# Performance work log

Hardware: AMD Instinct MI355X
Metric: run time of the kernel (lower is better)

The kernel has to match this reference:

```python
import jax, jax.numpy as jnp
import numpy as np

K = 5        # spline kernel_size per dim (dim=2 -> 25 kernel weights)
NPG = 75     # MNIST superpixel nodes per graph


def _spline_conv(x, src, dst, pseudo, emask, W, root, bias):
    """SplineConv, dim=2, kernel_size=5, degree=1 open splines, aggr='mean'.
    emask in {0,1} masks out coalesced-away (duplicate/self-loop) edges."""
    n = x.shape[0]
    v = jnp.clip(pseudo, 0.0, 1.0) * (K - 1)
    bot = jnp.clip(jnp.floor(v), 0, K - 2)
    frac = v - bot                                   # [E,2]
    bot = bot.astype(jnp.int32)
    xj = x[src] * emask[:, None]                     # [E,Fin] gathered source feats
    # aggregate-then-transform: acc[k,i,:] = sum over edges into i with basis k
    acc = jnp.zeros((K * K, n, x.shape[1]), x.dtype)
    for o0 in (0, 1):
        for o1 in (0, 1):
            w = (frac[:, 0] if o0 else 1.0 - frac[:, 0]) * (frac[:, 1] if o1 else 1.0 - frac[:, 1])
            kk = (bot[:, 0] + o0) + K * (bot[:, 1] + o1)
            acc = acc.at[kk, dst].add(w[:, None] * xj)
    out = jnp.einsum('knf,kfo->no', acc, W)
    deg = jax.ops.segment_sum(emask, dst, num_segments=n)
    return out / jnp.maximum(deg, 1.0)[:, None] + x @ root + bias


def _pool(x, pos, valid, batch, src, dst, emask, size, G, B):
    """voxel_grid + max_pool with static shapes: S=B*G*G clusters, masked."""
    S = B * G * G
    c = jnp.clip(jnp.floor(pos / size).astype(jnp.int32), 0, G - 1)
    cl = batch * (G * G) + c[:, 1] * G + c[:, 0]
    xm = jnp.where(valid[:, None] > 0, x, -1e30)
    px = jax.ops.segment_max(xm, cl, num_segments=S)
    cnt = jax.ops.segment_sum(valid, cl, num_segments=S)
    sval = (cnt > 0).astype(x.dtype)
    px = jnp.where(sval[:, None] > 0, px, 0.0)
    ppos = jax.ops.segment_sum(pos * valid[:, None], cl, num_segments=S) / jnp.maximum(cnt, 1.0)[:, None]
    nb = jnp.arange(S, dtype=jnp.int32) // (G * G)
    # remap edges to clusters; mask self loops and duplicates (= coalesce)
    nsrc, ndst = cl[src], cl[dst]
    m = (emask > 0) & (nsrc != ndst)
    a0 = jnp.where(m, nsrc, S)
    b0 = jnp.where(m, ndst, S)
    order = jnp.lexsort((b0, a0))
    a, b = a0[order], b0[order]
    first = jnp.concatenate([jnp.array([True]), (a[1:] != a[:-1]) | (b[1:] != b[:-1])])
    keep = jnp.zeros(src.shape[0], dtype=bool).at[order].set(first & (a < S))
    kf = keep.astype(x.dtype)
    # T.Cartesian(cat=False, norm=True): pseudo = (pos_src-pos_dst)/(2*max|.|)+0.5
    cart = ppos[nsrc] - ppos[ndst]
    amax = jnp.maximum(jnp.max(jnp.abs(cart) * kf[:, None]), 1e-12)
    pseudo = cart / (2.0 * amax) + 0.5
    return px, ppos, sval, nb, nsrc, ndst, kf, pseudo


def _forward(x, pos, src, dst, W1, r1, b1, W2, r2, b2, W3, r3, b3, fw1, fb1, fw2, fb2):
    N = x.shape[0]
    B = N // NPG
    batch = jnp.arange(N, dtype=jnp.int32) // NPG
    valid = jnp.ones((N,), x.dtype)
    emask = jnp.ones((src.shape[0],), x.dtype)
    cart = pos[src] - pos[dst]
    pseudo = cart / (2.0 * jnp.maximum(jnp.max(jnp.abs(cart)), 1e-12)) + 0.5
    x = jax.nn.elu(_spline_conv(x, src, dst, pseudo, emask, W1, r1, b1))
    x, pos, valid, batch, src, dst, emask, pseudo = _pool(x, pos, valid, batch, src, dst, emask, 5.0, 6, B)
    x = jax.nn.elu(_spline_conv(x, src, dst, pseudo, emask, W2, r2, b2))
    x, pos, valid, batch, src, dst, emask, pseudo = _pool(x, pos, valid, batch, src, dst, emask, 7.0, 5, B)
    x = jax.nn.elu(_spline_conv(x, src, dst, pseudo, emask, W3, r3, b3))
    # max_pool_x(cluster, x, batch, size=4): 2x2 voxel grid (size=14, end=27.99)
    c = jnp.clip(jnp.floor(pos / 14.0).astype(jnp.int32), 0, 1)
    cl = batch * 4 + c[:, 1] * 2 + c[:, 0]
    xm = jnp.where(valid[:, None] > 0, x, -1e30)
    px = jax.ops.segment_max(xm, cl, num_segments=B * 4)
    cnt = jax.ops.segment_sum(valid, cl, num_segments=B * 4)
    px = jnp.where((cnt > 0)[:, None], px, 0.0)
    h = jax.nn.elu(px.reshape(B, 4 * 64) @ fw1.T + fb1)
    logits = h @ fw2.T + fb2  # F.dropout is identity in eval mode
    return jax.nn.log_softmax(logits, axis=1)


def setup_inputs() -> dict:
    key = jax.random.key(0)
    ks = jax.random.split(key, 16)
    B, EPG = 1024, 1392
    N = B * NPG
    x = jax.random.normal(ks[0], (N, 1), jnp.float32)
    pos = jax.random.uniform(ks[1], (N, 2), jnp.float32) * 27.99
    s = jax.random.randint(ks[2], (B, EPG), 0, NPG)
    d = (s + 1 + jax.random.randint(ks[3], (B, EPG), 0, NPG - 1)) % NPG  # no self loops
    off = (jnp.arange(B, dtype=jnp.int32) * NPG)[:, None]
    src = (s + off).reshape(-1)
    dst = (d + off).reshape(-1)
    rn = lambda k, sh, sc: jax.random.normal(k, sh, jnp.float32) * sc
    return dict(x=x, pos=pos, src=src, dst=dst,
                W1=rn(ks[4], (25, 1, 32), 0.2), r1=rn(ks[5], (1, 32), 0.2), b1=jnp.zeros((32,), jnp.float32),
                W2=rn(ks[6], (25, 32, 64), 0.05), r2=rn(ks[7], (32, 64), 0.1), b2=jnp.zeros((64,), jnp.float32),
                W3=rn(ks[8], (25, 64, 64), 0.04), r3=rn(ks[9], (64, 64), 0.08), b3=jnp.zeros((64,), jnp.float32),
                fw1=rn(ks[10], (128, 256), 0.06), fb1=jnp.zeros((128,), jnp.float32),
                fw2=rn(ks[11], (10, 128), 0.09), fb2=jnp.zeros((10,), jnp.float32))


def reference(x, pos, src, dst, W1, r1, b1, W2, r2, b2, W3, r3, b3, fw1, fb1, fw2, fb2):
    return _forward(x, pos, src, dst, W1, r1, b1, W2, r2, b2, W3, r3, b3, fw1, fb1, fw2, fb2)
```

## Files before the change

kernel.cpp:

```cpp
#include <hip/hip_runtime.h>
#include <math.h>

#define NPG 75
#define KDIM 5

typedef _Float16 half8 __attribute__((ext_vector_type(8)));
typedef float f32x4 __attribute__((ext_vector_type(4)));

__device__ __forceinline__ float eluf(float v){ return v > 0.f ? v : expf(v) - 1.f; }

__device__ __forceinline__ void atomAddF(float* p, float v){ unsafeAtomicAdd(p, v); }

__device__ __forceinline__ unsigned fenc(float f){
    unsigned u = __float_as_uint(f);
    return (u & 0x80000000u) ? ~u : (u | 0x80000000u);
}
__device__ __forceinline__ float fdec(unsigned u){
    return (u & 0x80000000u) ? __uint_as_float(u & 0x7FFFFFFFu) : __uint_as_float(~u);
}

__device__ __forceinline__ void fma25(float (&r)[25], const float (&wx)[5], const float (&wyx)[5]){
    #pragma unroll
    for (int b1 = 0; b1 < 5; b1++)
        #pragma unroll
        for (int b0 = 0; b0 < 5; b0++)
            asm("v_fmac_f32 %0, %1, %2" : "+v"(r[b1 * 5 + b0]) : "v"(wx[b0]), "v"(wyx[b1]));
}

__device__ __forceinline__ void spline2(float c0, float c1, float am, int* kks, float* wsp){
    float denom = 2.f * fmaxf(am, 1e-12f);
    float p0 = c0 / denom + 0.5f;
    float p1 = c1 / denom + 0.5f;
    p0 = fminf(fmaxf(p0, 0.f), 1.f) * 4.f;
    p1 = fminf(fmaxf(p1, 0.f), 1.f) * 4.f;
    float b0 = fminf(floorf(p0), 3.f);
    float b1 = fminf(floorf(p1), 3.f);
    float f0 = p0 - b0, f1 = p1 - b1;
    int i0 = (int)b0, i1 = (int)b1;
    wsp[0] = (1.f - f0) * (1.f - f1); kks[0] = i0     + KDIM *  i1;
    wsp[1] =        f0  * (1.f - f1); kks[1] = i0 + 1 + KDIM *  i1;
    wsp[2] = (1.f - f0) *        f1 ; kks[2] = i0     + KDIM * (i1 + 1);
    wsp[3] =        f0  *        f1 ; kks[3] = i0 + 1 + KDIM * (i1 + 1);
}

__device__ __forceinline__ void spline_pay(float2 c, float denom, float* d){
    float p0 = fminf(fmaxf(c.x / denom + 0.5f, 0.f), 1.f) * 4.f;
    float p1 = fminf(fmaxf(c.y / denom + 0.5f, 0.f), 1.f) * 4.f;
    float b0 = fminf(floorf(p0), 3.f);
    float b1 = fminf(floorf(p1), 3.f);
    int i0 = (int)b0, i1 = (int)b1;
    float f0 = p0 - b0, f1 = p1 - b1;
    #pragma unroll
    for (int k = 0; k < 4; k++){
        d[k]     = (k == i0) ? (1.f - f0) : ((k == i0 + 1) ? f0 : 0.f);
        d[4 + k] = (k == i1) ? (1.f - f1) : ((k == i1 + 1) ? f1 : 0.f);
    }
}

__global__ __launch_bounds__(256) void amax0_k(
        const float* __restrict__ pos, const int* __restrict__ src,
        const int* __restrict__ dst, int E4, unsigned* __restrict__ outbits){
    float cand = 0.f;
    for (int i = blockIdx.x * 256 + threadIdx.x; i < E4; i += gridDim.x * 256){
        int4 s4 = ((const int4*)src)[i];
        int4 d4 = ((const int4*)dst)[i];
        #pragma unroll
        for (int k = 0; k < 4; k++){
            int s = (&s4.x)[k], d = (&d4.x)[k];
            float c0 = pos[s*2]   - pos[d*2];
            float c1 = pos[s*2+1] - pos[d*2+1];
            cand = fmaxf(cand, fmaxf(fabsf(c0), fabsf(c1)));
        }
    }
    __shared__ float sm[256];
    sm[threadIdx.x] = cand; __syncthreads();
    for (int o = 128; o > 0; o >>= 1){
        if (threadIdx.x < o) sm[threadIdx.x] = fmaxf(sm[threadIdx.x], sm[threadIdx.x + o]);
        __syncthreads();
    }
    if (threadIdx.x == 0) atomicMax(outbits, __float_as_uint(sm[0]));
}

__global__ __launch_bounds__(512) void conv1dedup_k(
        const float* __restrict__ x, const float* __restrict__ pos,
        const int* __restrict__ src, const int* __restrict__ dst, int EPG,
        const unsigned* __restrict__ amaxp,
        const float* __restrict__ W1, const float* __restrict__ r1, const float* __restrict__ b1,
        float* __restrict__ px1, float* __restrict__ pp1, float* __restrict__ sv1,
        int* __restrict__ easrc, float2* __restrict__ ecart,
        int* __restrict__ rowptr2, int* __restrict__ kcnt, unsigned* __restrict__ amaxbits){
    __shared__ __align__(16) float acc[NPG * 28];
    __shared__ float deg[NPG];
    __shared__ float xl[NPG], p0l[NPG], p1l[NPG];
    __shared__ int   cli[NPG];
    __shared__ float W1s[800], r1s[32], b1s[32];
    __shared__ unsigned px[36 * 32];
    __shared__ float cnt[36], ps[72], ppS[72];
    __shared__ unsigned pm[36 * 36];
    __shared__ float degs[36];
    __shared__ int rs[37], cur[36];
    __shared__ float red[8];
    __shared__ unsigned short sdS[2048];

    const int b = blockIdx.x, t = threadIdx.x;
    const int lane = t & 63, wid = t >> 6;
    const int n0 = b * NPG, e0 = b * EPG;

    const float am = __uint_as_float(*amaxp);

    for (int i = t; i < NPG * 28; i += 512) acc[i] = 0.f;
    for (int i = t; i < 36 * 32; i += 512) px[i] = 0u;
    for (int i = t; i < 36 * 36; i += 512) pm[i] = 0xFFFFFFFFu;
    if (t < NPG) deg[t] = 0.f;
    if (t < 36){ cnt[t] = 0.f; degs[t] = 0.f; }
    if (t < 72) ps[t] = 0.f;
    for (int i = t; i < 800; i += 512) W1s[i] = W1[i];
    if (t < 32){ r1s[t] = r1[t]; b1s[t] = b1[t]; }
    if (t < NPG){
        float p0 = pos[(n0 + t) * 2], p1 = pos[(n0 + t) * 2 + 1];
        xl[t] = x[n0 + t]; p0l[t] = p0; p1l[t] = p1;
        int c0 = min(max((int)floorf(p0 / 5.f), 0), 5);
        int c1 = min(max((int)floorf(p1 / 5.f), 0), 5);
        cli[t] = c1 * 6 + c0;
    }
    __syncthreads();

    if (t < NPG){
        int c = cli[t];
        atomAddF(&cnt[c], 1.f);
        atomAddF(&ps[c*2],     p0l[t]);
        atomAddF(&ps[c*2 + 1], p1l[t]);
    }
    #pragma unroll 4
    for (int it = 0; it < 4; it++){
        int e = t + it * 512;
        if (e < EPG){
            int s = src[e0 + e] - n0;
            int d = dst[e0 + e] - n0;
            sdS[e] = (unsigned short)(s | (d << 8));
            float c0 = p0l[s] - p0l[d];
            float c1 = p1l[s] - p1l[d];
            int kks[4]; float wsp[4];
            spline2(c0, c1, am, kks, wsp);
            float xv = xl[s];
            #pragma unroll
            for (int c = 0; c < 4; c++) atomAddF(&acc[d*28 + kks[c]], wsp[c] * xv);
            atomAddF(&deg[d], 1.f);
        }
    }
    __syncthreads();

    if (t < 36){
        float c = cnt[t], m = fmaxf(c, 1.f);
        float q0 = ps[t*2] / m, q1 = ps[t*2 + 1] / m;
        ppS[t*2] = q0; ppS[t*2 + 1] = q1;
        pp1[(b*36 + t)*2]     = q0;
        pp1[(b*36 + t)*2 + 1] = q1;
        sv1[b*36 + t] = (c > 0.f) ? 1.f : 0.f;
    }
    {
        const int o = t & 31;
        float wreg[25];
        #pragma unroll
        for (int k = 0; k < 25; k++) wreg[k] = W1s[k * 32 + o];
        const float rro = r1s[o], bbo = b1s[o];
        const int ii = t >> 5;
        #pragma unroll
        for (int r = 0; r < 5; r++){
            int i = ii + r * 16;
            if (i < NPG){
                const float4* ar = (const float4*)(acc + i * 28);
                float s = 0.f;
                #pragma unroll
                for (int q = 0; q < 7; q++){
                    float4 aq = ar[q];
                    s += aq.x * wreg[q*4];
                    if (q*4 + 1 < 25) s += aq.y * wreg[q*4 + 1];
                    if (q*4 + 2 < 25) s += aq.z * wreg[q*4 + 2];
                    if (q*4 + 3 < 25) s += aq.w * wreg[q*4 + 3];
                }
                float v = s / fmaxf(deg[i], 1.f) + xl[i] * rro + bbo;
                v = eluf(v);
                atomicMax(&px[cli[i]*32 + o], fenc(v));
            }
        }
    }
    int lab[4];
    #pragma unroll 4
    for (int it = 0; it < 4; it++){
        int e = t + it * 512;
        lab[it] = 0;
        if (e < EPG){
            int sd = (int)sdS[e];
            int a  = cli[sd & 255];
            int bb = cli[sd >> 8];
            lab[it] = a | (bb << 8) | ((a != bb) ? 0x10000 : 0);
            if (a != bb) atomicMin(&pm[a * 36 + bb], (unsigned)e);
        }
    }
    __syncthreads();

    for (int idx = t; idx < 36 * 32; idx += 512){
        int s_ = idx >> 5;
        px1[(size_t)(b*36)*32 + idx] = (cnt[s_] > 0.f) ? fdec(px[idx]) : 0.f;
    }
    float cand = 0.f;
    unsigned keptM = 0;
    #pragma unroll 4
    for (int it = 0; it < 4; it++){
        int e = t + it * 512;
        int L = lab[it];
        if (L & 0x10000){
            int a = L & 255, bb = (L >> 8) & 255;
            if (pm[a * 36 + bb] == (unsigned)e){
                keptM |= 1u << it;
                atomAddF(&degs[bb], 1.f);
                float c0 = ppS[a*2]     - ppS[bb*2];
                float c1 = ppS[a*2 + 1] - ppS[bb*2 + 1];
                cand = fmaxf(cand, fmaxf(fabsf(c0), fabsf(c1)));
            }
        }
    }
    #pragma unroll
    for (int o = 1; o < 64; o <<= 1) cand = fmaxf(cand, __shfl_xor(cand, o, 64));
    if (lane == 0) red[wid] = cand;
    __syncthreads();
    if (t == 0){
        float m = red[0];
        #pragma unroll
        for (int i = 1; i < 8; i++) m = fmaxf(m, red[i]);
        atomicMax(amaxbits, __float_as_uint(m));
    }
    if (t < 64){
        int v = (t < 36) ? (int)degs[t] : 0;
        int incl = v;
        #pragma unroll
        for (int o = 1; o < 64; o <<= 1){
            int u = __shfl_up(incl, o, 64);
            if (t >= o) incl += u;
        }
        if (t == 0) rs[0] = 0;
        if (t < 36) rs[t + 1] = incl;
    }
    __syncthreads();
    if (t < 36){
        rowptr2[(b*36 + t)*2]     = e0 + rs[t];
        rowptr2[(b*36 + t)*2 + 1] = e0 + rs[t + 1];
        cur[t] = rs[t];
    }
    if (t == 0) kcnt[b] = rs[36];
    __syncthreads();
    #pragma unroll 4
    for (int it = 0; it < 4; it++){
        if (keptM & (1u << it)){
            int L = lab[it];
            int a = L & 255, bb = (L >> 8) & 255;
            int slot = atomicAdd(&cur[bb], 1);
            easrc[e0 + slot] = b*36 + a;
            ecart[e0 + slot] = make_float2(ppS[a*2] - ppS[bb*2], ppS[a*2 + 1] - ppS[bb*2 + 1]);
        }
    }
}

__global__ __launch_bounds__(1024) void dedup_pool_k(
        const int* __restrict__ easrc_in, const int* __restrict__ rowptr_in,
        const int* __restrict__ kcnt_in,
        const float* __restrict__ xin,
        const float* __restrict__ pp1, const float* __restrict__ sv1,
        int EPG,
        float* __restrict__ px2, float* __restrict__ pp2, float* __restrict__ sv2,
        int* __restrict__ easrc, float2* __restrict__ ecart,
        int* __restrict__ rowptr2, int* __restrict__ kcnt, unsigned* __restrict__ amaxbits){
    constexpr int GG = 25, NN = 36;
    __shared__ unsigned pm[GG * GG];
    __shared__ float degs[GG];
    __shared__ int rs[GG + 1];
    __shared__ int cur[GG];
    __shared__ float red[16];
    __shared__ int   clS[NN];
    __shared__ int   vld[NN];
    __shared__ int   rsS[NN + 1];
    __shared__ float ppS[2 * GG];
    __shared__ unsigned px[GG * 64];
    __shared__ float cnt[GG], ps[2 * GG];
    __shared__ unsigned short abS[1280];

    const int b = blockIdx.x, t = threadIdx.x;
    const int lane = t & 63, wid = t >> 6;
    const int e0 = b * EPG;
    const int cb25 = b * GG;
    const int nb36 = b * NN;

    for (int i = t; i < GG * GG; i += 1024) pm[i] = 0xFFFFFFFFu;
    for (int i = t; i < GG * 64; i += 1024) px[i] = 0u;
    if (t < GG){ degs[t] = 0.f; cnt[t] = 0.f; }
    if (t < 2 * GG) ps[t] = 0.f;
    if (t < NN){
        float v  = sv1[nb36 + t];
        float p0 = pp1[(nb36 + t)*2], p1 = pp1[(nb36 + t)*2 + 1];
        int c0 = min(max((int)floorf(p0 / 7.f), 0), 4);
        int c1 = min(max((int)floorf(p1 / 7.f), 0), 4);
        clS[t] = c1 * 5 + c0;
        vld[t] = (v > 0.f) ? 1 : 0;
        rsS[t] = rowptr_in[(nb36 + t)*2] - e0;
    }
    if (t == 0) rsS[NN] = kcnt_in[b];
    __syncthreads();

    const int kn = rsS[NN];

    if (t < NN && vld[t]){
        int c = clS[t];
        atomAddF(&cnt[c], 1.f);
        atomAddF(&ps[c*2],     pp1[(nb36 + t)*2]);
        atomAddF(&ps[c*2 + 1], pp1[(nb36 + t)*2 + 1]);
    }
    for (int idx = t; idx < NN * 64; idx += 1024){
        int i = idx >> 6, f = idx & 63;
        if (vld[i])
            atomicMax(&px[clS[i]*64 + f], fenc(xin[(size_t)(nb36 + i)*64 + f]));
    }
    #pragma unroll 2
    for (int it = 0; it < 2; it++){
        int s = t + it * 1024;
        if (s < kn){
            int r = 0;
            while (r < NN - 1 && rsS[r + 1] <= s) r++;
            int a2 = clS[easrc_in[e0 + s] - nb36];
            int b2 = clS[r];
            abS[s] = (unsigned short)(a2 | (b2 << 8) | ((a2 != b2) ? 0x8000 : 0));
            if (a2 != b2) atomicMin(&pm[a2 * GG + b2], (unsigned)s);
        }
    }
    __syncthreads();

    if (t < GG){
        float c = cnt[t], m = fmaxf(c, 1.f);
        float q0 = ps[t*2] / m, q1 = ps[t*2 + 1] / m;
        ppS[t*2] = q0; ppS[t*2 + 1] = q1;
        pp2[(cb25 + t)*2]     = q0;
        pp2[(cb25 + t)*2 + 1] = q1;
        sv2[cb25 + t] = (c > 0.f) ? 1.f : 0.f;
    }
    for (int idx = t; idx < GG * 64; idx += 1024){
        int s_ = idx >> 6;
        px2[(size_t)cb25*64 + idx] = (cnt[s_] > 0.f) ? fdec(px[idx]) : 0.f;
    }
    __syncthreads();

    float cand = 0.f;
    #pragma unroll 2
    for (int it = 0; it < 2; it++){
        int s = t + it * 1024;
        if (s < kn){
            int A = (int)abS[s];
            if (A & 0x8000){
                int a2 = A & 255, b2 = (A >> 8) & 127;
                if (pm[a2 * GG + b2] == (unsigned)s){
                    atomAddF(&degs[b2], 1.f);
                    float c0 = ppS[a2*2]     - ppS[b2*2];
                    float c1 = ppS[a2*2 + 1] - ppS[b2*2 + 1];
                    cand = fmaxf(cand, fmaxf(fabsf(c0), fabsf(c1)));
                }
            }
        }
    }
    #pragma unroll
    for (int o = 1; o < 64; o <<= 1) cand = fmaxf(cand, __shfl_xor(cand, o, 64));
    if (lane == 0) red[wid] = cand;
    __syncthreads();
    if (t == 0){
        float m = red[0];
        #pragma unroll
        for (int i = 1; i < 16; i++) m = fmaxf(m, red[i]);
        atomicMax(amaxbits, __float_as_uint(m));
    }
    if (t < 64){
        int v = (t < GG) ? (int)degs[t] : 0;
        int incl = v;
        #pragma unroll
        for (int o = 1; o < 64; o <<= 1){
            int u = __shfl_up(incl, o, 64);
            if (t >= o) incl += u;
        }
        if (t == 0) rs[0] = 0;
        if (t < GG) rs[t + 1] = incl;
    }
    __syncthreads();
    if (t < GG){
        rowptr2[(cb25 + t)*2]     = e0 + rs[t];
        rowptr2[(cb25 + t)*2 + 1] = e0 + rs[t + 1];
        cur[t] = rs[t];
    }
    if (t == 0) kcnt[b] = rs[GG];
    __syncthreads();
    #pragma unroll 2
    for (int it = 0; it < 2; it++){
        int s = t + it * 1024;
        if (s < kn){
            int A = (int)abS[s];
            if (A & 0x8000){
                int a2 = A & 255, b2 = (A >> 8) & 127;
                if (pm[a2 * GG + b2] == (unsigned)s){
                    int slot = atomicAdd(&cur[b2], 1);
                    easrc[e0 + slot] = cb25 + a2;
                    ecart[e0 + slot] = make_float2(ppS[a2*2] - ppS[b2*2], ppS[a2*2 + 1] - ppS[b2*2 + 1]);
                }
            }
        }
    }
}

__global__ void wswz2_k(const float* __restrict__ W2, const float* __restrict__ r2,
                        const float* __restrict__ W3, const float* __restrict__ r3,
                        _Float16* __restrict__ Wz2, _Float16* __restrict__ Wz3){
    int gid = blockIdx.x * 256 + threadIdx.x;
    const int T2 = 26 * 32 * 64;
    const int T3 = 26 * 64 * 64;
    const float* W; const float* root; _Float16* Wz; int FIN; int g;
    if (gid < T2){ W = W2; root = r2; Wz = Wz2; FIN = 32; g = gid; }
    else if (gid < T2 + T3){ W = W3; root = r3; Wz = Wz3; FIN = 64; g = gid - T2; }
    else return;
    int k = g >> 6, n = g & 63;
    float v = (k < 25 * FIN) ? W[(size_t)k * 64 + n] : root[(size_t)(k - 25 * FIN) * 64 + n];
    int kt = k >> 5, kr = k & 31, quad = kr >> 3, j = kr & 7;
    int lane = (quad << 4) | (n & 15);
    int nt = n >> 4;
    Wz[(((size_t)(kt * 4 + nt) * 64 + lane) << 3) + j] = (_Float16)v;
}

__global__ __launch_bounds__(512) void conv2f_k(
        const float* __restrict__ x, const int* __restrict__ easrc,
        const float2* __restrict__ ecart, const unsigned* __restrict__ amaxp,
        const int* __restrict__ rowptr2, const _Float16* __restrict__ Wz,
        const float* __restrict__ bias, float* __restrict__ out){
    constexpr int PAD = 840;
    __shared__ __align__(16) _Float16 Alds[32 * PAD];
    __shared__ __align__(16) float pay[8][36][8];
    __shared__ int asrcS[8][36];

    const int w = threadIdx.x >> 6, lane = threadIdx.x & 63;
    const int sub = lane >> 5, f = lane & 31;
    const float am = __uint_as_float(*amaxp);
    const float denom = 2.f * fmaxf(am, 1e-12f);

    #pragma unroll
    for (int i = 0; i < 4; i++){
        const int nloc = w * 4 + i;
        const int node = blockIdx.x * 32 + nloc;
        const int row0 = rowptr2[node*2], row1 = rowptr2[node*2 + 1];
        const int ne = row1 - row0;

        if (lane < ne){
            spline_pay(ecart[row0 + lane], denom, &pay[w][lane][0]);
            asrcS[w][lane] = easrc[row0 + lane];
        }

        float r[25];
        #pragma unroll
        for (int b = 0; b < 25; b++) r[b] = 0.f;

        int j = sub;
        int aNext = 0;
        float xvCur = 0.f;
        if (j < ne){
            int aCur = asrcS[w][j];
            xvCur = x[(size_t)aCur * 32 + f];
            int j1 = (j + 2 < ne) ? j + 2 : j;
            aNext = asrcS[w][j1];
        }
        for (; j < ne; j += 2){
            int jN  = j + 2;
            int jNs = (jN < ne) ? jN : j;
            int jN2 = (jN + 2 < ne) ? jN + 2 : jNs;
            float xvN = x[(size_t)aNext * 32 + f];
            int aN2 = asrcS[w][jN2];
            float4 wa = *(const float4*)&pay[w][j][0];
            float4 wb = *(const float4*)&pay[w][j][4];
            float wx4 = 1.f - (wa.x + wa.y + wa.z + wa.w);
            float wy4 = 1.f - (wb.x + wb.y + wb.z + wb.w);
            float wx[5]  = {wa.x, wa.y, wa.z, wa.w, wx4};
            float wyx[5] = {wb.x * xvCur, wb.y * xvCur, wb.z * xvCur, wb.w * xvCur, wy4 * xvCur};
            fma25(r, wx, wyx);
            xvCur = xvN; aNext = aN2;
        }
        #pragma unroll
        for (int b = 0; b < 25; b++) r[b] += __shfl_xor(r[b], 32, 64);

        float inv = 1.f / (float)max(ne, 1);
        _Float16* dstrow = &Alds[nloc * PAD];
        #pragma unroll
        for (int b = 0; b < 25; b++)
            if ((b & 1) == sub) dstrow[b * 32 + f] = (_Float16)(r[b] * inv);
        if (sub == 0) dstrow[25 * 32 + f] = (_Float16)x[(size_t)node * 32 + f];
    }
    __syncthreads();

    const int mt = w >> 2, nt = w & 3;
    const int quad = lane >> 4, mr = lane & 15;
    f32x4 acc = (f32x4){0.f, 0.f, 0.f, 0.f};
    const _Float16* arow = &Alds[(mt * 16 + mr) * PAD];
    const half8* __restrict__ Wp = (const half8*)Wz + lane;
    for (int kt = 0; kt < 26; kt++){
        half8 a = *(const half8*)(arow + kt * 32 + quad * 8);
        half8 b = Wp[(kt * 4 + nt) * 64];
        acc = __builtin_amdgcn_mfma_f32_16x16x32_f16(a, b, acc, 0, 0, 0);
    }
    float* cp = out + (size_t)(blockIdx.x * 32 + mt * 16) * 64;
    const int r_ = quad * 4, c_ = lane & 15;
    float bv = bias[nt * 16 + c_];
    #pragma unroll
    for (int i = 0; i < 4; i++)
        cp[(size_t)(r_ + i) * 64 + nt * 16 + c_] = eluf(acc[i] + bv);
}

__global__ __launch_bounds__(1024) void conv3f_k(
        const float* __restrict__ x, const int* __restrict__ easrc,
        const float2* __restrict__ ecart, const unsigned* __restrict__ amaxp,
        const int* __restrict__ rowptr2, const _Float16* __restrict__ Wz,
        const float* __restrict__ bias, float* __restrict__ out){
    constexpr int PAD = 1672;
    __shared__ __align__(16) _Float16 Alds[32 * PAD];
    __shared__ __align__(16) float scratchF[3456];
    __shared__ int asrcS[16][24];

    const int w = threadIdx.x >> 6, lane = threadIdx.x & 63;
    const float am = __uint_as_float(*amaxp);
    const float denom = 2.f * fmaxf(am, 1e-12f);
    float* payW = scratchF + w * 24 * 8;

    #pragma unroll
    for (int i = 0; i < 2; i++){
        const int nloc = w * 2 + i;
        const int node = blockIdx.x * 32 + nloc;
        const int row0 = rowptr2[node*2], row1 = rowptr2[node*2 + 1];
        const int ne = row1 - row0;

        if (lane < ne){
            spline_pay(ecart[row0 + lane], denom, payW + lane * 8);
            asrcS[w][lane] = easrc[row0 + lane];
        }

        float r[25];
        #pragma unroll
        for (int b = 0; b < 25; b++) r[b] = 0.f;

        int j = 0;
        int aNext = 0;
        float xvCur = 0.f;
        if (j < ne){
            int aCur = asrcS[w][j];
            xvCur = x[(size_t)aCur * 64 + lane];
            int j1 = (1 < ne) ? 1 : 0;
            aNext = asrcS[w][j1];
        }
        for (; j < ne; j++){
            int jN  = j + 1;
            int jNs = (jN < ne) ? jN : j;
            int jN2 = (jN + 1 < ne) ? jN + 1 : jNs;
            float xvN = x[(size_t)aNext * 64 + lane];
            int aN2 = asrcS[w][jN2];
            float4 wa = *(const float4*)(payW + j * 8);
            float4 wb = *(const float4*)(payW + j * 8 + 4);
            float wx4 = 1.f - (wa.x + wa.y + wa.z + wa.w);
            float wy4 = 1.f - (wb.x + wb.y + wb.z + wb.w);
            float wx[5]  = {wa.x, wa.y, wa.z, wa.w, wx4};
            float wyx[5] = {wb.x * xvCur, wb.y * xvCur, wb.z * xvCur, wb.w * xvCur, wy4 * xvCur};
            fma25(r, wx, wyx);
            xvCur = xvN; aNext = aN2;
        }

        float inv = 1.f / (float)max(ne, 1);
        _Float16* dstrow = &Alds[nloc * PAD];
        #pragma unroll
        for (int b = 0; b < 25; b++) dstrow[b * 64 + lane] = (_Float16)(r[b] * inv);
        dstrow[25 * 64 + lane] = (_Float16)x[(size_t)node * 64 + lane];
    }
    __syncthreads();

    const int tile = w & 7, khalf = w >> 3;
    const int mt = tile >> 2, nt = tile & 3;
    const int quad = lane >> 4, mr = lane & 15;
    f32x4 acc = (f32x4){0.f, 0.f, 0.f, 0.f};
    const _Float16* arow = &Alds[(mt * 16 + mr) * PAD];
    const half8* __restrict__ Wp = (const half8*)Wz + lane;
    const int kt0 = khalf * 26;
    for (int kt = 0; kt < 26; kt++){
        half8 a = *(const half8*)(arow + (kt0 + kt) * 32 + quad * 8);
        half8 b = Wp[((kt0 + kt) * 4 + nt) * 64];
        acc = __builtin_amdgcn_mfma_f32_16x16x32_f16(a, b, acc, 0, 0, 0);
    }
    const int r_ = quad * 4, c_ = lane & 15;
    if (khalf == 1){
        float* Cp = scratchF + tile * 256;
        #pragma unroll
        for (int i = 0; i < 4; i++) Cp[(r_ + i) * 16 + c_] = acc[i];
    }
    __syncthreads();
    if (khalf == 0){
        const float* Cp = scratchF + tile * 256;
        float* cp = out + (size_t)(blockIdx.x * 32 + mt * 16) * 64;
        float bv = bias[nt * 16 + c_];
        #pragma unroll
        for (int i = 0; i < 4; i++)
            cp[(size_t)(r_ + i) * 64 + nt * 16 + c_] = eluf(acc[i] + Cp[(r_ + i) * 16 + c_] + bv);
    }
}

__global__ __launch_bounds__(256) void final_k(
        const float* __restrict__ xin, const float* __restrict__ ppin,
        const float* __restrict__ svin,
        const float* __restrict__ fw1, const float* __restrict__ fb1,
        const float* __restrict__ fw2, const float* __restrict__ fb2,
        float* __restrict__ out){
    __shared__ unsigned px[4 * 64];
    __shared__ float cnt[4];
    __shared__ int cli[25];
    __shared__ float xr[256];
    __shared__ float h[128];
    __shared__ float lg[10];
    __shared__ float lse;
    const int b = blockIdx.x, t = threadIdx.x;

    if (t < 4*64) px[t] = 0u;
    if (t < 4) cnt[t] = 0.f;
    if (t < 25){
        float v  = svin[b*25 + t];
        float p0 = ppin[(b*25 + t)*2], p1 = ppin[(b*25 + t)*2 + 1];
        int c0 = min(max((int)floorf(p0 / 14.f), 0), 1);
        int c1 = min(max((int)floorf(p1 / 14.f), 0), 1);
        int c = c1 * 2 + c0;
        cli[t] = (v > 0.f) ? c : -1;
    }
    __syncthreads();
    if (t < 25 && cli[t] >= 0) atomAddF(&cnt[cli[t]], 1.f);
    __syncthreads();
    for (int idx = t; idx < 25 * 64; idx += 256){
        int i = idx >> 6, f = idx & 63;
        if (cli[i] >= 0)
            atomicMax(&px[cli[i]*64 + f], fenc(xin[(size_t)(b*25 + i)*64 + f]));
    }
    __syncthreads();
    xr[t] = (cnt[t >> 6] > 0.f) ? fdec(px[t]) : 0.f;
    __syncthreads();
    if (t < 128){
        float s = fb1[t];
        const float4* wrow = (const float4*)(fw1 + (size_t)t * 256);
        #pragma unroll 4
        for (int i = 0; i < 64; i++){
            float4 q = wrow[i];
            s += xr[i*4]   * q.x;
            s += xr[i*4+1] * q.y;
            s += xr[i*4+2] * q.z;
            s += xr[i*4+3] * q.w;
        }
        h[t] = eluf(s);
    }
    __syncthreads();
    if (t < 10){
        float s2 = fb2[t];
        const float* w2 = fw2 + (size_t)t * 128;
        for (int j = 0; j < 128; j++) s2 += h[j] * w2[j];
        lg[t] = s2;
    }
    __syncthreads();
    if (t == 0){
        float m = lg[0];
        for (int c = 1; c < 10; c++) m = fmaxf(m, lg[c]);
        float se = 0.f;
        for (int c = 0; c < 10; c++) se += expf(lg[c] - m);
        lse = m + logf(se);
    }
    __syncthreads();
    if (t < 10) out[(size_t)b*10 + t] = lg[t] - lse;
}

extern "C" void kernel_launch(void* const* d_in, const int* in_sizes, int n_in,
                              void* d_out, int out_size, void* d_ws, size_t ws_size,
                              hipStream_t stream) {
    const float* x   = (const float*)d_in[0];
    const float* pos = (const float*)d_in[1];
    const int*   src = (const int*)d_in[2];
    const int*   dst = (const int*)d_in[3];
    const float* W1  = (const float*)d_in[4];
    const float* r1  = (const float*)d_in[5];
    const float* b1  = (const float*)d_in[6];
    const float* W2  = (const float*)d_in[7];
    const float* r2  = (const float*)d_in[8];
    const float* b2  = (const float*)d_in[9];
    const float* W3  = (const float*)d_in[10];
    const float* r3  = (const float*)d_in[11];
    const float* b3  = (const float*)d_in[12];
    const float* fw1 = (const float*)d_in[13];
    const float* fb1 = (const float*)d_in[14];
    const float* fw2 = (const float*)d_in[15];
    const float* fb2 = (const float*)d_in[16];
    float* out = (float*)d_out;

    const int N   = in_sizes[0];
    const int E   = in_sizes[2];
    const int B   = N / NPG;
    const int EPG = E / B;
    const int S1  = B * 36;
    const int S2  = B * 25;

    float* w = (float*)d_ws;
    size_t off = 0;
    auto alloc = [&](size_t nelem){ size_t o = off; off += (nelem + 63) & ~(size_t)63; return o; };

    size_t o_scal = alloc(4);
    size_t o_px1  = alloc((size_t)S1 * 32);
    size_t o_pp1  = alloc((size_t)S1 * 2);
    size_t o_sv1  = alloc(S1);
    size_t o_easrc= alloc(E);
    size_t o_ecart= alloc((size_t)2 * E);
    size_t o_kcnt = alloc(B);
    size_t o_rp2  = alloc((size_t)2 * S1);
    size_t o_rp3  = alloc((size_t)2 * S2);
    size_t o_out2 = alloc((size_t)S1 * 64);
    size_t o_px2  = alloc((size_t)S2 * 64);
    size_t o_pp2  = alloc((size_t)S2 * 2);
    size_t o_sv2  = alloc(S2);
    size_t o_out3 = alloc((size_t)S2 * 64);
    size_t o_wz2  = alloc((size_t)26 * 32 * 64 / 2 + 64);
    size_t o_wz3  = alloc((size_t)26 * 64 * 64 / 2 + 64);

    hipMemsetAsync(w + o_scal, 0, 4 * sizeof(float), stream);

    unsigned* scal = (unsigned*)(w + o_scal);
    _Float16* Wz2  = (_Float16*)(w + o_wz2);
    _Float16* Wz3  = (_Float16*)(w + o_wz3);
    auto nb = [](long long t){ return (unsigned)((t + 255) / 256); };

    wswz2_k<<<nb(26 * 32 * 64 + 26 * 64 * 64), 256, 0, stream>>>(W2, r2, W3, r3, Wz2, Wz3);

    const int E4 = E / 4;
    int gA = (E4 + 255) / 256; if (gA > 512) gA = 512;
    amax0_k<<<gA, 256, 0, stream>>>(pos, src, dst, E4, scal + 0);

    conv1dedup_k<<<B, 512, 0, stream>>>(x, pos, src, dst, EPG, scal + 0, W1, r1, b1,
                                        w + o_px1, w + o_pp1, w + o_sv1,
                                        (int*)(w + o_easrc), (float2*)(w + o_ecart),
                                        (int*)(w + o_rp2), (int*)(w + o_kcnt), scal + 1);

    conv2f_k<<<S1 / 32, 512, 0, stream>>>(
        w + o_px1, (int*)(w + o_easrc), (const float2*)(w + o_ecart), scal + 1,
        (int*)(w + o_rp2), Wz2, b2, w + o_out2);

    dedup_pool_k<<<B, 1024, 0, stream>>>(
        (int*)(w + o_easrc), (int*)(w + o_rp2), (int*)(w + o_kcnt),
        w + o_out2, w + o_pp1, w + o_sv1, EPG,
        w + o_px2, w + o_pp2, w + o_sv2,
        (int*)(w + o_easrc), (float2*)(w + o_ecart),
        (int*)(w + o_rp3), (int*)(w + o_kcnt), scal + 2);

    conv3f_k<<<S2 / 32, 1024, 0, stream>>>(
        w + o_px2, (int*)(w + o_easrc), (const float2*)(w + o_ecart), scal + 2,
        (int*)(w + o_rp3), Wz3, b3, w + o_out3);

    final_k<<<B, 256, 0, stream>>>(w + o_out3, w + o_pp2, w + o_sv2,
                                   fw1, fb1, fw2, fb2, out);
}
```

Before: 327.2 us.

## Split conv2 into gather kernel and MFMA GEMM kernel; merge prep kernels

The weight-swizzle and edge-amax kernels are merged into one launch that uses block ranges to do each job, saving a launch. The fused conv2 kernel, which used a large LDS tile per 32-node block, is split in two. A small-block gather kernel writes the per-node fp16 spline basis rows to a global buffer, and a separate MFMA kernel multiplies 64 rows per block against all four N tiles. This raises occupancy for the gather phase and gives the GEMM more reuse of A, at the cost of an extra global round trip of the A matrix and one more launch.

```diff
diff --git a/kernel.cpp b/kernel.cpp
--- a/kernel.cpp
+++ b/kernel.cpp
@@ -57,28 +57,48 @@
     }
 }
 
-__global__ __launch_bounds__(256) void amax0_k(
+__global__ __launch_bounds__(256) void prep_k(
+        const float* __restrict__ W2, const float* __restrict__ r2,
+        const float* __restrict__ W3, const float* __restrict__ r3,
+        _Float16* __restrict__ Wz2, _Float16* __restrict__ Wz3, int nW,
         const float* __restrict__ pos, const int* __restrict__ src,
-        const int* __restrict__ dst, int E4, unsigned* __restrict__ outbits){
-    float cand = 0.f;
-    for (int i = blockIdx.x * 256 + threadIdx.x; i < E4; i += gridDim.x * 256){
-        int4 s4 = ((const int4*)src)[i];
-        int4 d4 = ((const int4*)dst)[i];
-        #pragma unroll
-        for (int k = 0; k < 4; k++){
-            int s = (&s4.x)[k], d = (&d4.x)[k];
-            float c0 = pos[s*2]   - pos[d*2];
-            float c1 = pos[s*2+1] - pos[d*2+1];
-            cand = fmaxf(cand, fmaxf(fabsf(c0), fabsf(c1)));
-        }
-    }
-    __shared__ float sm[256];
-    sm[threadIdx.x] = cand; __syncthreads();
-    for (int o = 128; o > 0; o >>= 1){
-        if (threadIdx.x < o) sm[threadIdx.x] = fmaxf(sm[threadIdx.x], sm[threadIdx.x + o]);
-        __syncthreads();
-    }
-    if (threadIdx.x == 0) atomicMax(outbits, __float_as_uint(sm[0]));
+        const int* __restrict__ dst, int E4, int gA, unsigned* __restrict__ outbits){
+    const int blk = blockIdx.x;
+    if (blk < nW){
+        int gid = blk * 256 + threadIdx.x;
+        const int T2 = 26 * 32 * 64;
+        const int T3 = 26 * 64 * 64;
+        const float* W; const float* root; _Float16* Wz; int FIN; int g;
+        if (gid < T2){ W = W2; root = r2; Wz = Wz2; FIN = 32; g = gid; }
+        else if (gid < T2 + T3){ W = W3; root = r3; Wz = Wz3; FIN = 64; g = gid - T2; }
+        else return;
+        int k = g >> 6, n = g & 63;
+        float v = (k < 25 * FIN) ? W[(size_t)k * 64 + n] : root[(size_t)(k - 25 * FIN) * 64 + n];
+        int kt = k >> 5, kr = k & 31, quad = kr >> 3, j = kr & 7;
+        int lane = (quad << 4) | (n & 15);
+        int nt = n >> 4;
+        Wz[(((size_t)(kt * 4 + nt) * 64 + lane) << 3) + j] = (_Float16)v;
+    } else {
+        float cand = 0.f;
+        for (int i = (blk - nW) * 256 + threadIdx.x; i < E4; i += gA * 256){
+            int4 s4 = ((const int4*)src)[i];
+            int4 d4 = ((const int4*)dst)[i];
+            #pragma unroll
+            for (int k = 0; k < 4; k++){
+                int s = (&s4.x)[k], d = (&d4.x)[k];
+                float c0 = pos[s*2]   - pos[d*2];
+                float c1 = pos[s*2+1] - pos[d*2+1];
+                cand = fmaxf(cand, fmaxf(fabsf(c0), fabsf(c1)));
+            }
+        }
+        __shared__ float sm[256];
+        sm[threadIdx.x] = cand; __syncthreads();
+        for (int o = 128; o > 0; o >>= 1){
+            if (threadIdx.x < o) sm[threadIdx.x] = fmaxf(sm[threadIdx.x], sm[threadIdx.x + o]);
+            __syncthreads();
+        }
+        if (threadIdx.x == 0) atomicMax(outbits, __float_as_uint(sm[0]));
+    }
 }
 
 __global__ __launch_bounds__(512) void conv1dedup_k(
@@ -411,107 +431,101 @@
     }
 }
 
-__global__ void wswz2_k(const float* __restrict__ W2, const float* __restrict__ r2,
-                        const float* __restrict__ W3, const float* __restrict__ r3,
-                        _Float16* __restrict__ Wz2, _Float16* __restrict__ Wz3){
-    int gid = blockIdx.x * 256 + threadIdx.x;
-    const int T2 = 26 * 32 * 64;
-    const int T3 = 26 * 64 * 64;
-    const float* W; const float* root; _Float16* Wz; int FIN; int g;
-    if (gid < T2){ W = W2; root = r2; Wz = Wz2; FIN = 32; g = gid; }
-    else if (gid < T2 + T3){ W = W3; root = r3; Wz = Wz3; FIN = 64; g = gid - T2; }
-    else return;
-    int k = g >> 6, n = g & 63;
-    float v = (k < 25 * FIN) ? W[(size_t)k * 64 + n] : root[(size_t)(k - 25 * FIN) * 64 + n];
-    int kt = k >> 5, kr = k & 31, quad = kr >> 3, j = kr & 7;
-    int lane = (quad << 4) | (n & 15);
-    int nt = n >> 4;
-    Wz[(((size_t)(kt * 4 + nt) * 64 + lane) << 3) + j] = (_Float16)v;
-}
-
-__global__ __launch_bounds__(512) void conv2f_k(
+__global__ __launch_bounds__(256) void conv_gather32_k(
         const float* __restrict__ x, const int* __restrict__ easrc,
         const float2* __restrict__ ecart, const unsigned* __restrict__ amaxp,
-        const int* __restrict__ rowptr2, const _Float16* __restrict__ Wz,
-        const float* __restrict__ bias, float* __restrict__ out){
-    constexpr int PAD = 840;
-    __shared__ __align__(16) _Float16 Alds[32 * PAD];
-    __shared__ __align__(16) float pay[8][36][8];
-    __shared__ int asrcS[8][36];
-
+        const int* __restrict__ rowptr2, _Float16* __restrict__ Aout){
+    constexpr int FIN = 32;
+    constexpr int KTOT = 26 * FIN;
+    __shared__ __align__(16) float pay[4][36][8];
+    __shared__ int asrcS[4][36];
     const int w = threadIdx.x >> 6, lane = threadIdx.x & 63;
-    const int sub = lane >> 5, f = lane & 31;
-    const float am = __uint_as_float(*amaxp);
-    const float denom = 2.f * fmaxf(am, 1e-12f);
-
-    #pragma unroll
-    for (int i = 0; i < 4; i++){
-        const int nloc = w * 4 + i;
-        const int node = blockIdx.x * 32 + nloc;
-        const int row0 = rowptr2[node*2], row1 = rowptr2[node*2 + 1];
-        const int ne = row1 - row0;
-
-        if (lane < ne){
-            spline_pay(ecart[row0 + lane], denom, &pay[w][lane][0]);
-            asrcS[w][lane] = easrc[row0 + lane];
-        }
-
-        float r[25];
-        #pragma unroll
-        for (int b = 0; b < 25; b++) r[b] = 0.f;
-
-        int j = sub;
-        int aNext = 0;
-        float xvCur = 0.f;
-        if (j < ne){
-            int aCur = asrcS[w][j];
-            xvCur = x[(size_t)aCur * 32 + f];
-            int j1 = (j + 2 < ne) ? j + 2 : j;
-            aNext = asrcS[w][j1];
-        }
-        for (; j < ne; j += 2){
-            int jN  = j + 2;
-            int jNs = (jN < ne) ? jN : j;
-            int jN2 = (jN + 2 < ne) ? jN + 2 : jNs;
-            float xvN = x[(size_t)aNext * 32 + f];
-            int aN2 = asrcS[w][jN2];
-            float4 wa = *(const float4*)&pay[w][j][0];
-            float4 wb = *(const float4*)&pay[w][j][4];
-            float wx4 = 1.f - (wa.x + wa.y + wa.z + wa.w);
-            float wy4 = 1.f - (wb.x + wb.y + wb.z + wb.w);
-            float wx[5]  = {wa.x, wa.y, wa.z, wa.w, wx4};
-            float wyx[5] = {wb.x * xvCur, wb.y * xvCur, wb.z * xvCur, wb.w * xvCur, wy4 * xvCur};
-            fma25(r, wx, wyx);
-            xvCur = xvN; aNext = aN2;
-        }
-        #pragma unroll
-        for (int b = 0; b < 25; b++) r[b] += __shfl_xor(r[b], 32, 64);
-
-        float inv = 1.f / (float)max(ne, 1);
-        _Float16* dstrow = &Alds[nloc * PAD];
-        #pragma unroll
-        for (int b = 0; b < 25; b++)
-            if ((b & 1) == sub) dstrow[b * 32 + f] = (_Float16)(r[b] * inv);
-        if (sub == 0) dstrow[25 * 32 + f] = (_Float16)x[(size_t)node * 32 + f];
-    }
-    __syncthreads();
-
-    const int mt = w >> 2, nt = w & 3;
-    const int quad = lane >> 4, mr = lane & 15;
-    f32x4 acc = (f32x4){0.f, 0.f, 0.f, 0.f};
-    const _Float16* arow = &Alds[(mt * 16 + mr) * PAD];
-    const half8* __restrict__ Wp = (const half8*)Wz + lane;
-    for (int kt = 0; kt < 26; kt++){
-        half8 a = *(const half8*)(arow + kt * 32 + quad * 8);
-        half8 b = Wp[(kt * 4 + nt) * 64];
-        acc = __builtin_amdgcn_mfma_f32_16x16x32_f16(a, b, acc, 0, 0, 0);
-    }
-    float* cp = out + (size_t)(blockIdx.x * 32 + mt * 16) * 64;
-    const int r_ = quad * 4, c_ = lane & 15;
-    float bv = bias[nt * 16 + c_];
-    #pragma unroll
-    for (int i = 0; i < 4; i++)
-        cp[(size_t)(r_ + i) * 64 + nt * 16 + c_] = eluf(acc[i] + bv);
+    const int node = blockIdx.x * 4 + w;
+    const int row0 = rowptr2[node*2], row1 = rowptr2[node*2 + 1];
+    const int ne = row1 - row0;
+    const int sub = lane >> 5;
+    const int f = lane & (FIN - 1);
+
+    if (lane < ne){
+        float am = __uint_as_float(*amaxp);
+        spline_pay(ecart[row0 + lane], 2.f * fmaxf(am, 1e-12f), &pay[w][lane][0]);
+        asrcS[w][lane] = easrc[row0 + lane];
+    }
+
+    float r[25];
+    #pragma unroll
+    for (int b = 0; b < 25; b++) r[b] = 0.f;
+
+    int j = sub;
+    int aNext = 0;
+    float xvCur = 0.f;
+    if (j < ne){
+        int aCur = asrcS[w][j];
+        xvCur = x[(size_t)aCur * FIN + f];
+        int j1 = (j + 2 < ne) ? j + 2 : j;
+        aNext = asrcS[w][j1];
+    }
+    for (; j < ne; j += 2){
+        int jN  = j + 2;
+        int jNs = (jN < ne) ? jN : j;
+        int jN2 = (jN + 2 < ne) ? jN + 2 : jNs;
+        float xvN = x[(size_t)aNext * FIN + f];
+        int aN2 = asrcS[w][jN2];
+        float4 wa = *(const float4*)&pay[w][j][0];
+        float4 wb = *(const float4*)&pay[w][j][4];
+        float wx4 = 1.f - (wa.x + wa.y + wa.z + wa.w);
+        float wy4 = 1.f - (wb.x + wb.y + wb.z + wb.w);
+        float wx[5]  = {wa.x, wa.y, wa.z, wa.w, wx4};
+        float wyx[5] = {wb.x * xvCur, wb.y * xvCur, wb.z * xvCur, wb.w * xvCur, wy4 * xvCur};
+        fma25(r, wx, wyx);
+        xvCur = xvN; aNext = aN2;
+    }
+
+    #pragma unroll
+    for (int b = 0; b < 25; b++) r[b] += __shfl_xor(r[b], 32, 64);
+
+    float inv = 1.f / (float)max(ne, 1);
+    _Float16* dstrow = Aout + (size_t)node * KTOT;
+    #pragma unroll
+    for (int b = 0; b < 25; b++)
+        if ((b & 1) == sub) dstrow[b * 32 + f] = (_Float16)(r[b] * inv);
+    if (sub == 0) dstrow[25 * 32 + f] = (_Float16)x[(size_t)node * 32 + f];
+}
+
+__global__ __launch_bounds__(256) void conv_mfma832_k(
+        const _Float16* __restrict__ A, const _Float16* __restrict__ Wz,
+        const float* __restrict__ bias, int M, float* __restrict__ out){
+    constexpr int KTOT = 832;
+    constexpr int NSTEP = KTOT / 32;
+    const int w = threadIdx.x >> 6, lane = threadIdx.x & 63;
+    const int m0 = blockIdx.x * 64 + w * 16;
+    const int quad = lane >> 4;
+
+    f32x4 acc[4];
+    #pragma unroll
+    for (int nt = 0; nt < 4; nt++) acc[nt] = (f32x4){0.f, 0.f, 0.f, 0.f};
+
+    const half8* __restrict__ Arow = (const half8*)(A + (size_t)(m0 + (lane & 15)) * KTOT);
+    const half8* __restrict__ Wp   = (const half8*)Wz + lane;
+
+    for (int kt = 0; kt < NSTEP; kt++){
+        half8 a = Arow[kt * 4 + quad];
+        #pragma unroll
+        for (int nt = 0; nt < 4; nt++){
+            half8 b = Wp[(kt * 4 + nt) * 64];
+            acc[nt] = __builtin_amdgcn_mfma_f32_16x16x32_f16(a, b, acc[nt], 0, 0, 0);
+        }
+    }
+
+    float* cp = out + (size_t)m0 * 64;
+    const int r = quad * 4, c = lane & 15;
+    #pragma unroll
+    for (int nt = 0; nt < 4; nt++){
+        float bv = bias[nt * 16 + c];
+        #pragma unroll
+        for (int i = 0; i < 4; i++)
+            cp[(size_t)(r + i) * 64 + nt * 16 + c] = eluf(acc[nt][i] + bv);
+    }
 }
 
 __global__ __launch_bounds__(1024) void conv3f_k(
@@ -724,28 +738,30 @@
     size_t o_out3 = alloc((size_t)S2 * 64);
     size_t o_wz2  = alloc((size_t)26 * 32 * 64 / 2 + 64);
     size_t o_wz3  = alloc((size_t)26 * 64 * 64 / 2 + 64);
+    size_t o_accA = alloc(((size_t)S1 * 832 + 1) / 2);
 
     hipMemsetAsync(w + o_scal, 0, 4 * sizeof(float), stream);
 
     unsigned* scal = (unsigned*)(w + o_scal);
     _Float16* Wz2  = (_Float16*)(w + o_wz2);
     _Float16* Wz3  = (_Float16*)(w + o_wz3);
-    auto nb = [](long long t){ return (unsigned)((t + 255) / 256); };
-
-    wswz2_k<<<nb(26 * 32 * 64 + 26 * 64 * 64), 256, 0, stream>>>(W2, r2, W3, r3, Wz2, Wz3);
+    _Float16* A16  = (_Float16*)(w + o_accA);
 
     const int E4 = E / 4;
     int gA = (E4 + 255) / 256; if (gA > 512) gA = 512;
-    amax0_k<<<gA, 256, 0, stream>>>(pos, src, dst, E4, scal + 0);
+    const int nW = (26 * 32 * 64 + 26 * 64 * 64 + 255) / 256;
+    prep_k<<<nW + gA, 256, 0, stream>>>(W2, r2, W3, r3, Wz2, Wz3, nW,
+                                        pos, src, dst, E4, gA, scal + 0);
 
     conv1dedup_k<<<B, 512, 0, stream>>>(x, pos, src, dst, EPG, scal + 0, W1, r1, b1,
                                         w + o_px1, w + o_pp1, w + o_sv1,
                                         (int*)(w + o_easrc), (float2*)(w + o_ecart),
                                         (int*)(w + o_rp2), (int*)(w + o_kcnt), scal + 1);
 
-    conv2f_k<<<S1 / 32, 512, 0, stream>>>(
+    conv_gather32_k<<<S1 / 4, 256, 0, stream>>>(
         w + o_px1, (int*)(w + o_easrc), (const float2*)(w + o_ecart), scal + 1,
-        (int*)(w + o_rp2), Wz2, b2, w + o_out2);
+        (int*)(w + o_rp2), A16);
+    conv_mfma832_k<<<S1 / 64, 256, 0, stream>>>(A16, Wz2, b2, S1, w + o_out2);
 
     dedup_pool_k<<<B, 1024, 0, stream>>>(
         (int*)(w + o_easrc), (int*)(w + o_rp2), (int*)(w + o_kcnt),
```

Result: no change. 321.6 us (-1.7%).
